# Kernel optimization log

Hardware: AMD Instinct MI355X
Metric: run time of the kernel (lower is better)

## Reference

```python
import jax, jax.numpy as jnp
import numpy as np

N_E = 1024
N_H = 16
SZ = N_E // N_H  # 64
NEG_INF = float('-inf')


def _layernorm(x, g, b):
    # Faithful to source: unbiased variance (ddof=1), eps added AFTER sqrt.
    mu = jnp.mean(x, axis=-1, keepdims=True)
    v = jnp.var(x, axis=-1, keepdims=True, ddof=1)
    xn = (x - mu) / (jnp.sqrt(v) + 1e-8)
    return g * xn + b


def setup_inputs() -> dict:
    key = jax.random.key(0)
    ks = jax.random.split(key, 16)
    s = 0.02
    x = jax.random.normal(ks[0], (4, 2048, N_E), dtype=jnp.float32)
    # Stacked per-head Q/K/V linears: weight [H, sz, n_e], bias [H, sz]
    Wq = jax.random.normal(ks[1], (N_H, SZ, N_E), dtype=jnp.float32) * s
    bq = jax.random.normal(ks[2], (N_H, SZ), dtype=jnp.float32) * s
    Wk = jax.random.normal(ks[3], (N_H, SZ, N_E), dtype=jnp.float32) * s
    bk = jax.random.normal(ks[4], (N_H, SZ), dtype=jnp.float32) * s
    Wv = jax.random.normal(ks[5], (N_H, SZ, N_E), dtype=jnp.float32) * s
    bv = jax.random.normal(ks[6], (N_H, SZ), dtype=jnp.float32) * s
    Wo = jax.random.normal(ks[7], (N_E, N_E), dtype=jnp.float32) * s
    bo = jax.random.normal(ks[8], (N_E,), dtype=jnp.float32) * s
    g1 = jnp.ones((N_E,), dtype=jnp.float32)
    be1 = jnp.zeros((N_E,), dtype=jnp.float32)
    g2 = jnp.ones((N_E,), dtype=jnp.float32)
    be2 = jnp.zeros((N_E,), dtype=jnp.float32)
    W1 = jax.random.normal(ks[9], (4 * N_E, N_E), dtype=jnp.float32) * s
    bf1 = jax.random.normal(ks[10], (4 * N_E,), dtype=jnp.float32) * s
    W2 = jax.random.normal(ks[11], (N_E, 4 * N_E), dtype=jnp.float32) * s
    bf2 = jax.random.normal(ks[12], (N_E,), dtype=jnp.float32) * s
    return dict(x=x, Wq=Wq, bq=bq, Wk=Wk, bk=bk, Wv=Wv, bv=bv, Wo=Wo, bo=bo,
                g1=g1, be1=be1, g2=g2, be2=be2, W1=W1, bf1=bf1, W2=W2, bf2=bf2)


def reference(x, Wq, bq, Wk, bk, Wv, bv, Wo, bo, g1, be1, g2, be2, W1, bf1, W2, bf2):
    # --- MHA sublayer ---
    xn = _layernorm(x, g1, be1)
    # Q/K/V for all heads at once: [B, H, S, sz]
    Q = jnp.einsum('bsd,hkd->bhsk', xn, Wq) + bq[None, :, None, :]
    K = jnp.einsum('bsd,hkd->bhsk', xn, Wk) + bk[None, :, None, :]
    V = jnp.einsum('bsd,hkd->bhsk', xn, Wv) + bv[None, :, None, :]
    scores = jnp.einsum('bhqk,bhmk->bhqm', Q, K) / (SZ ** 0.5)  # [B,H,S,S]
    # Faithful to source quirk: mask where tril(scores) == 0
    masked = jnp.where(jnp.tril(scores) == 0, NEG_INF, scores)
    attn = jax.nn.softmax(masked, axis=-1)
    o = jnp.einsum('bhqm,bhmk->bhqk', attn, V)  # [B,H,S,sz]
    B, H, S, _ = o.shape
    o = jnp.transpose(o, (0, 2, 1, 3)).reshape(B, S, H * SZ)  # concat heads
    x = x + o @ Wo.T + bo
    # --- FFN sublayer (dropout = identity in eval) ---
    xn2 = _layernorm(x, g2, be2)
    h = jax.nn.gelu(xn2 @ W1.T + bf1, approximate=False)
    x = x + h @ W2.T + bf2
    return x
```

## Files before the change

### kernel.cpp

```cpp
#include <hip/hip_runtime.h>
#include <math.h>


typedef unsigned short u16;
typedef unsigned int u32;
typedef __attribute__((ext_vector_type(8))) short bf16x8;
typedef __attribute__((ext_vector_type(4))) float f32x4;

#define T_TOK 8192
#define DM    1024
#define SEQ   2048

__device__ __forceinline__ u16 f2bf(float f) {
  union { float f; unsigned int u; } c; c.f = f;
  unsigned int u = c.u + 0x7fffu + ((c.u >> 16) & 1u);
  return (u16)(u >> 16);
}

__device__ __forceinline__ u32 pk2(float a, float b) {
  return (u32)f2bf(a) | ((u32)f2bf(b) << 16);
}

__device__ __forceinline__ float bf2f(short s) {
  union { float f; unsigned int u; } c; c.u = ((u32)(u16)s) << 16;
  return c.f;
}

__device__ __forceinline__ void gload16(const void* gp, void* lp) {
  __builtin_amdgcn_global_load_lds(
      (const __attribute__((address_space(1))) void*)gp,
      (__attribute__((address_space(3))) void*)lp, 16, 0, 0);
}

__global__ __launch_bounds__(256) void cast_all(const float* __restrict__ Wq,
    const float* __restrict__ Wk, const float* __restrict__ Wv,
    const float* __restrict__ Wo, const float* __restrict__ W1,
    const float* __restrict__ W2, u16* __restrict__ WqkvB,
    u16* __restrict__ WoB, u16* __restrict__ W1B, u16* __restrict__ W2B) {
  for (int i = blockIdx.x * 256 + threadIdx.x; i < 3145728; i += gridDim.x * 256) {
    const float* s; u16* d; int j;
    if (i < 262144)       { s = Wq; d = WqkvB;           j = i; }
    else if (i < 524288)  { s = Wk; d = WqkvB + 1048576; j = i - 262144; }
    else if (i < 786432)  { s = Wv; d = WqkvB + 2097152; j = i - 524288; }
    else if (i < 1048576) { s = Wo; d = WoB;             j = i - 786432; }
    else if (i < 2097152) { s = W1; d = W1B;             j = i - 1048576; }
    else                  { s = W2; d = W2B;             j = i - 2097152; }
    float4 v = reinterpret_cast<const float4*>(s)[j];
    ushort4 o = { f2bf(v.x), f2bf(v.y), f2bf(v.z), f2bf(v.w) };
    reinterpret_cast<ushort4*>(d)[j] = o;
  }
}

__global__ __launch_bounds__(256) void concat_bias(const float* __restrict__ q,
    const float* __restrict__ k, const float* __restrict__ v, float* __restrict__ out) {
  int i = blockIdx.x * 256 + threadIdx.x;
  float val = (i < 1024) ? q[i] : (i < 2048) ? k[i - 1024] : v[i - 2048];
  out[i] = val;
}

__global__ __launch_bounds__(256) void ln_kernel(const float* __restrict__ x,
    const float* __restrict__ g, const float* __restrict__ b, u16* __restrict__ out) {
  __shared__ float red[4];
  const int tid = threadIdx.x, l = tid & 63, w = tid >> 6;
  const size_t row = blockIdx.x;
  float4 v = reinterpret_cast<const float4*>(x + row * DM)[tid];
  float s = v.x + v.y + v.z + v.w;
#pragma unroll
  for (int off = 1; off < 64; off <<= 1) s += __shfl_xor(s, off, 64);
  if (l == 0) red[w] = s;
  __syncthreads();
  float mu = (red[0] + red[1] + red[2] + red[3]) * (1.0f / 1024.0f);
  float dx = v.x - mu, dy = v.y - mu, dz = v.z - mu, dw = v.w - mu;
  float ss = dx * dx + dy * dy + dz * dz + dw * dw;
#pragma unroll
  for (int off = 1; off < 64; off <<= 1) ss += __shfl_xor(ss, off, 64);
  __syncthreads();
  if (l == 0) red[w] = ss;
  __syncthreads();
  float var = (red[0] + red[1] + red[2] + red[3]) * (1.0f / 1023.0f);
  float inv = 1.0f / (sqrtf(var) + 1e-8f);
  const int c = tid * 4;
  u16* o = out + row * DM + c;
  o[0] = f2bf(dx * inv * g[c + 0] + b[c + 0]);
  o[1] = f2bf(dy * inv * g[c + 1] + b[c + 1]);
  o[2] = f2bf(dz * inv * g[c + 2] + b[c + 2]);
  o[3] = f2bf(dw * inv * g[c + 3] + b[c + 3]);
}

__global__ __launch_bounds__(256) void vt_kernel(const u16* __restrict__ vr,
                                                 u16* __restrict__ vt) {
  __shared__ u16 t[64][72];
  const int st = blockIdx.x;
  const int bh = blockIdx.y, b = bh >> 4, h = bh & 15;
  const int tid = threadIdx.x;
  const int ss = tid >> 3, dc = (tid & 7) * 8;
  const u16* src = vr + (size_t)(b * SEQ + st * 64) * 1024 + h * 64;
  *(bf16x8*)&t[ss][dc]      = *(const bf16x8*)(src + (size_t)ss * 1024 + dc);
  *(bf16x8*)&t[ss + 32][dc] = *(const bf16x8*)(src + (size_t)(ss + 32) * 1024 + dc);
  __syncthreads();
  const int d0 = tid >> 3, s0 = (tid & 7) * 8;
  u16* dst = vt + (size_t)bh * 64 * SEQ + st * 64;
  bf16x8 o0, o1;
#pragma unroll
  for (int i = 0; i < 8; ++i) {
    o0[i] = (short)t[s0 + i][d0];
    o1[i] = (short)t[s0 + i][d0 + 32];
  }
  *(bf16x8*)(dst + (size_t)d0 * SEQ + s0)        = o0;
  *(bf16x8*)(dst + (size_t)(d0 + 32) * SEQ + s0) = o1;
}

template <int EPI, int BM>
__global__ __launch_bounds__(512) void gemm8p(const u16* __restrict__ A,
    const u16* __restrict__ Bw, const float* __restrict__ bias,
    const float* res, void* Cout, void* aux, int M, int N, int K, int gx) {
  constexpr int MI  = BM / 32;
  constexpr int AMI = MI / 2;
  constexpr int VC  = (BM == 256) ? 6 : 5;
  __shared__ __align__(16) u16 ldsA[2][2][BM * 32];
  __shared__ __align__(16) u16 ldsB[2][2][256 * 32];
  const int tid = threadIdx.x;
  const int l = tid & 63;
  const int w = tid >> 6;
  const int wm = w >> 2, wn = w & 3;
  const int lr = l & 15, lg = l >> 4;

  const int nb = gridDim.x;
  const int q = nb >> 3, r = nb & 7;
  const int xcd = blockIdx.x & 7, jj = blockIdx.x >> 3;
  const int lid = (xcd < r ? xcd * (q + 1) : r * (q + 1) + (xcd - r) * q) + jj;
  const int stid = lid >> 5, pos = lid & 31;
  const int nstx = gx >> 2;
  const int stx = stid % nstx, sty = stid / nstx;
  const int bx = stx * 4 + (pos & 3), by = sty * 8 + (pos >> 2);
  const int m0 = by * BM, n0 = bx * 256;

  const int Dl = tid * 16;
  const int Ls = Dl ^ (((Dl >> 7) & 3) << 4);
  const int srow = Ls >> 6;
  const int scol = (Ls & 63) >> 1;
  const u16* aS0 = A  + (size_t)(m0 + srow) * K + scol;
  const u16* aS1 = aS0 + (size_t)128 * K;
  const u16* bS0 = Bw + (size_t)(n0 + srow) * K + scol;
  const u16* bS1 = bS0 + (size_t)128 * K;

  const int sx = ((lr >> 1) & 3) << 4;
  const int aBase = (wm * (BM / 2) + lr) * 64 + ((lg * 16) ^ sx);
  const int bBase = (wn * 64 + lr) * 64 + ((lg * 16) ^ sx);

  f32x4 acc[MI][4];
#pragma unroll
  for (int i = 0; i < MI; ++i)
#pragma unroll
    for (int j = 0; j < 4; ++j) acc[i][j] = f32x4{0.f, 0.f, 0.f, 0.f};
  bf16x8 bv[2][4];

  const int NT = K >> 6;
  const int NI = NT >> 1;

  auto stA = [&](int d, int ks, int tile) {
    u16* dst = &ldsA[d][ks][tid * 8];
    const int ko = tile * 64 + ks * 32;
    gload16(aS0 + ko, dst);
    if constexpr (BM == 256) gload16(aS1 + ko, dst + 4096);
  };
  auto stB = [&](int d, int ks, int tile) {
    u16* dst = &ldsB[d][ks][tid * 8];
    const int ko = tile * 64 + ks * 32;
    gload16(bS0 + ko, dst);
    gload16(bS1 + ko, dst + 4096);
  };

  stB(0, 0, 0); stB(0, 1, 0); stA(0, 0, 0); stA(0, 1, 0);
  stB(1, 0, 1); stB(1, 1, 1); stA(1, 0, 1);
  asm volatile("s_waitcnt vmcnt(%0)" :: "i"(VC) : "memory");
  __builtin_amdgcn_sched_barrier(0);
  __builtin_amdgcn_s_barrier();

#define PHASE(DBUF, KS, MH, READB, STAGE, ENDV)                               \
  {                                                                           \
    const char* abuf = (const char*)&ldsA[DBUF][KS][0];                       \
    const char* bbuf = (const char*)&ldsB[DBUF][KS][0];                       \
    bf16x8 av[AMI];                                                           \
    _Pragma("unroll")                                                         \
    for (int i = 0; i < AMI; ++i)                                             \
      av[i] = *(const bf16x8*)(abuf + aBase + ((MH) * AMI + i) * 1024);       \
    if (READB) {                                                              \
      _Pragma("unroll")                                                       \
      for (int ni = 0; ni < 4; ++ni)                                          \
        bv[KS][ni] = *(const bf16x8*)(bbuf + bBase + ni * 1024);              \
    }                                                                         \
    STAGE;                                                                    \
    __builtin_amdgcn_s_barrier();                                             \
    asm volatile("s_waitcnt lgkmcnt(0)" ::: "memory");                        \
    __builtin_amdgcn_sched_barrier(0);                                        \
    __builtin_amdgcn_s_setprio(1);                                            \
    _Pragma("unroll")                                                         \
    for (int i = 0; i < AMI; ++i)                                             \
      _Pragma("unroll")                                                       \
      for (int ni = 0; ni < 4; ++ni)                                          \
        acc[(MH) * AMI + i][ni] = __builtin_amdgcn_mfma_f32_16x16x32_bf16(    \
            av[i], bv[KS][ni], acc[(MH) * AMI + i][ni], 0, 0, 0);             \
    __builtin_amdgcn_s_setprio(0);                                            \
    ENDV;                                                                     \
    __builtin_amdgcn_s_barrier();                                             \
  }

#define ENDV_CNT                                                              \
  {                                                                           \
    if (t + 1 < NI) {                                                         \
      asm volatile("s_waitcnt vmcnt(%0)" :: "i"(VC) : "memory");              \
    } else {                                                                  \
      asm volatile("s_waitcnt vmcnt(0)" ::: "memory");                        \
    }                                                                         \
    __builtin_amdgcn_sched_barrier(0);                                        \
  }

  for (int t = 0; t < NI; ++t) {
    const int t2 = 2 * t;
    const bool s0 = (t2 + 2 < NT);
    const bool s1 = (t2 + 3 < NT);
    PHASE(0, 0, 0, 1, { stA(1, 1, t2 + 1); }, {});
    PHASE(0, 1, 0, 1, { if (s0) stB(0, 0, t2 + 2); }, {});
    PHASE(0, 0, 1, 0, { if (s0) stB(0, 1, t2 + 2); }, {});
    PHASE(0, 1, 1, 0, { if (s0) stA(0, 0, t2 + 2); }, ENDV_CNT);
    PHASE(1, 0, 0, 1, { if (s0) stA(0, 1, t2 + 2); }, {});
    PHASE(1, 1, 0, 1, { if (s1) stB(1, 0, t2 + 3); }, {});
    PHASE(1, 0, 1, 0, { if (s1) stB(1, 1, t2 + 3); }, {});
    PHASE(1, 1, 1, 0, { if (s1) stA(1, 0, t2 + 3); }, ENDV_CNT);
  }
#undef PHASE
#undef ENDV_CNT

  float bs[4];
#pragma unroll
  for (int ni = 0; ni < 4; ++ni) bs[ni] = bias[n0 + wn * 64 + ni * 16 + lr];
#pragma unroll
  for (int mi = 0; mi < MI; ++mi) {
#pragma unroll
    for (int j = 0; j < 4; ++j) {
      const int rr = m0 + wm * (BM / 2) + mi * 16 + lg * 4 + j;
#pragma unroll
      for (int ni = 0; ni < 4; ++ni) {
        const int c = n0 + wn * 64 + ni * 16 + lr;
        float v = acc[mi][ni][j] + bs[ni];
        if constexpr (EPI == 0) {
          if (n0 >= 2048) {
            ((u16*)aux)[(size_t)rr * 1024 + (c - 2048)] = f2bf(v);
          } else {
            ((u16*)Cout)[(size_t)rr * 2048 + c] = f2bf(v);
          }
        } else if constexpr (EPI == 1) {
          const size_t idx = (size_t)rr * N + c;
          ((float*)Cout)[idx] = v + res[idx];
        } else {
          const size_t idx = (size_t)rr * N + c;
          float gv = 0.5f * v * (1.0f + erff(v * 0.70710678118654752f));
          ((u16*)Cout)[idx] = f2bf(gv);
        }
      }
    }
  }
}

__global__ __launch_bounds__(512) void attn_kernel(const u16* __restrict__ qk,
    const u16* __restrict__ vt, u16* __restrict__ obuf) {
  __shared__ __align__(16) u16 ldsK[64 * 64];
  __shared__ __align__(16) u16 ldsV[64 * 64];
  __shared__ __align__(16) u16 ldsP[8][2][16 * 72];
  const int tid = threadIdx.x, l = tid & 63, w = tid >> 6;
  const int lr = l & 15, lg = l >> 4;
  const int bx = blockIdx.x;
  const int bh = blockIdx.y, b = bh >> 4, h = bh & 15;
  const u16* qbase = qk + (size_t)b * SEQ * 2048 + h * 64;
  const u16* kbase = qk + (size_t)b * SEQ * 2048 + 1024 + h * 64;
  const u16* vbase = vt + (size_t)bh * 64 * SEQ;

  const int srow = tid >> 3;
  const int scb  = ((tid & 7) * 16) ^ ((srow & 7) << 4);
  const int sel  = scb >> 1;

#pragma unroll
  for (int half = 0; half < 2; ++half) {
    const int qt = half ? (7 - bx) : bx;
    const int q0 = qt * 256 + w * 32;
    bf16x8 qf[2][2];
#pragma unroll
    for (int mi = 0; mi < 2; ++mi)
#pragma unroll
      for (int ks = 0; ks < 2; ++ks) {
        bf16x8 raw = *(const bf16x8*)(qbase +
            (size_t)(q0 + mi * 16 + lr) * 2048 + ks * 32 + lg * 8);
        bf16x8 sc8;
#pragma unroll
        for (int i = 0; i < 8; ++i) sc8[i] = (short)f2bf(bf2f(raw[i]) * 0.125f);
        qf[mi][ks] = sc8;
      }

    f32x4 o[2][4];
#pragma unroll
    for (int mi = 0; mi < 2; ++mi)
#pragma unroll
      for (int nd = 0; nd < 4; ++nd) o[mi][nd] = f32x4{0.f, 0.f, 0.f, 0.f};
    float m_[2] = {-1e30f, -1e30f}, ls[2] = {0.f, 0.f};

    const int nt = 4 * qt + 4;
    const int qmaxw = q0 + 31;

    for (int kt = 0; kt < nt; ++kt) {
      gload16(kbase + (size_t)(kt * 64 + srow) * 2048 + sel, &ldsK[tid * 8]);
      gload16(vbase + (size_t)srow * SEQ + kt * 64 + sel,    &ldsV[tid * 8]);
      __syncthreads();

      if (kt * 64 <= qmaxw) {
        f32x4 sc[2][4];
#pragma unroll
        for (int mi = 0; mi < 2; ++mi)
#pragma unroll
          for (int ni = 0; ni < 4; ++ni) sc[mi][ni] = f32x4{0.f, 0.f, 0.f, 0.f};
#pragma unroll
        for (int ks = 0; ks < 2; ++ks)
#pragma unroll
          for (int ni = 0; ni < 4; ++ni) {
            const int r2 = ni * 16 + lr;
            const int cb = (r2 << 7) + ((ks * 64 + lg * 16) ^ ((r2 & 7) << 4));
            bf16x8 kf = *(const bf16x8*)&ldsK[cb >> 1];
            sc[0][ni] = __builtin_amdgcn_mfma_f32_16x16x32_bf16(kf, qf[0][ks], sc[0][ni], 0, 0, 0);
            sc[1][ni] = __builtin_amdgcn_mfma_f32_16x16x32_bf16(kf, qf[1][ks], sc[1][ni], 0, 0, 0);
          }

        if (kt * 64 + 63 > q0) {
#pragma unroll
          for (int mi = 0; mi < 2; ++mi) {
            const int qa = q0 + mi * 16 + lr;
#pragma unroll
            for (int ni = 0; ni < 4; ++ni)
#pragma unroll
              for (int j = 0; j < 4; ++j) {
                const int ka = kt * 64 + ni * 16 + lg * 4 + j;
                if (ka > qa) sc[mi][ni][j] = -1e30f;
              }
          }
        }

#pragma unroll
        for (int mi = 0; mi < 2; ++mi) {
          float mx = sc[mi][0][0];
#pragma unroll
          for (int ni = 0; ni < 4; ++ni)
#pragma unroll
            for (int j = 0; j < 4; ++j) mx = fmaxf(mx, sc[mi][ni][j]);
          mx = fmaxf(mx, __shfl_xor(mx, 16, 64));
          mx = fmaxf(mx, __shfl_xor(mx, 32, 64));
          const float newm = fmaxf(m_[mi], mx);
          const float alpha = __expf(m_[mi] - newm);
          m_[mi] = newm;
          float ps = 0.f;
#pragma unroll
          for (int ni = 0; ni < 4; ++ni) {
            float p0 = __expf(sc[mi][ni][0] - newm);
            float p1 = __expf(sc[mi][ni][1] - newm);
            float p2 = __expf(sc[mi][ni][2] - newm);
            float p3 = __expf(sc[mi][ni][3] - newm);
            ps += (p0 + p1) + (p2 + p3);
            u32 w0 = pk2(p0, p1), w1 = pk2(p2, p3);
            *(uint2*)&ldsP[w][mi][lr * 72 + ni * 16 + lg * 4] = make_uint2(w0, w1);
          }
          ps += __shfl_xor(ps, 16, 64);
          ps += __shfl_xor(ps, 32, 64);
          ls[mi] = ls[mi] * alpha + ps;
          const float a0 = __shfl(alpha, lg * 4 + 0, 16);
          const float a1 = __shfl(alpha, lg * 4 + 1, 16);
          const float a2 = __shfl(alpha, lg * 4 + 2, 16);
          const float a3 = __shfl(alpha, lg * 4 + 3, 16);
#pragma unroll
          for (int nd = 0; nd < 4; ++nd) {
            o[mi][nd][0] *= a0; o[mi][nd][1] *= a1;
            o[mi][nd][2] *= a2; o[mi][nd][3] *= a3;
          }
        }

#pragma unroll
        for (int ks = 0; ks < 2; ++ks) {
          bf16x8 pf0 = *(const bf16x8*)&ldsP[w][0][lr * 72 + ks * 32 + lg * 8];
          bf16x8 pf1 = *(const bf16x8*)&ldsP[w][1][lr * 72 + ks * 32 + lg * 8];
#pragma unroll
          for (int nd = 0; nd < 4; ++nd) {
            const int r2 = nd * 16 + lr;
            const int cb = (r2 << 7) + ((ks * 64 + lg * 16) ^ ((r2 & 7) << 4));
            bf16x8 vf = *(const bf16x8*)&ldsV[cb >> 1];
            o[0][nd] = __builtin_amdgcn_mfma_f32_16x16x32_bf16(pf0, vf, o[0][nd], 0, 0, 0);
            o[1][nd] = __builtin_amdgcn_mfma_f32_16x16x32_bf16(pf1, vf, o[1][nd], 0, 0, 0);
          }
        }
      }
      __syncthreads();
    }

#pragma unroll
    for (int mi = 0; mi < 2; ++mi) {
      const float i0 = 1.0f / __shfl(ls[mi], lg * 4 + 0, 16);
      const float i1 = 1.0f / __shfl(ls[mi], lg * 4 + 1, 16);
      const float i2 = 1.0f / __shfl(ls[mi], lg * 4 + 2, 16);
      const float i3 = 1.0f / __shfl(ls[mi], lg * 4 + 3, 16);
      const int qrow = q0 + mi * 16 + lg * 4;
#pragma unroll
      for (int nd = 0; nd < 4; ++nd) {
        const int d = nd * 16 + lr;
        u16* op = obuf + (size_t)(b * SEQ + qrow) * DM + h * 64 + d;
        op[0 * DM] = f2bf(o[mi][nd][0] * i0);
        op[1 * DM] = f2bf(o[mi][nd][1] * i1);
        op[2 * DM] = f2bf(o[mi][nd][2] * i2);
        op[3 * DM] = f2bf(o[mi][nd][3] * i3);
      }
    }
  }
}

extern "C" void kernel_launch(void* const* d_in, const int* in_sizes, int n_in,
                              void* d_out, int out_size, void* d_ws, size_t ws_size,
                              hipStream_t stream) {
  const float* x   = (const float*)d_in[0];
  const float* Wq  = (const float*)d_in[1];
  const float* bq  = (const float*)d_in[2];
  const float* Wk  = (const float*)d_in[3];
  const float* bk  = (const float*)d_in[4];
  const float* Wv  = (const float*)d_in[5];
  const float* bv  = (const float*)d_in[6];
  const float* Wo  = (const float*)d_in[7];
  const float* bo  = (const float*)d_in[8];
  const float* g1  = (const float*)d_in[9];
  const float* be1 = (const float*)d_in[10];
  const float* g2  = (const float*)d_in[11];
  const float* be2 = (const float*)d_in[12];
  const float* W1  = (const float*)d_in[13];
  const float* bf1 = (const float*)d_in[14];
  const float* W2  = (const float*)d_in[15];
  const float* bf2 = (const float*)d_in[16];
  float* out = (float*)d_out;

  char* ws = (char*)d_ws;
  size_t off = 0;
  auto alloc = [&](size_t bytes) {
    char* p = ws + off;
    off += (bytes + 255) & ~(size_t)255;
    return p;
  };
  u16* xnB = (u16*)alloc((size_t)T_TOK * DM * 2);
  u16* D    = (u16*)alloc((size_t)T_TOK * 4096 * 2);
  u16* qkB  = D;
  u16* VTg  = D + (size_t)T_TOK * 2048;
  u16* Vrow = D + (size_t)T_TOK * 3072;
  u16* oB   = Vrow;
  u16* HB   = D;
  u16*   WqkvB = (u16*)alloc((size_t)3072 * 1024 * 2);
  u16*   WoB   = (u16*)alloc((size_t)1024 * 1024 * 2);
  u16*   W1B   = (u16*)alloc((size_t)4096 * 1024 * 2);
  u16*   W2B   = (u16*)alloc((size_t)1024 * 4096 * 2);
  float* bqkv  = (float*)alloc(3072 * 4);

  cast_all<<<2048, 256, 0, stream>>>(Wq, Wk, Wv, Wo, W1, W2,
                                     WqkvB, WoB, W1B, W2B);
  concat_bias<<<12, 256, 0, stream>>>(bq, bk, bv, bqkv);

  ln_kernel<<<T_TOK, 256, 0, stream>>>(x, g1, be1, xnB);
  gemm8p<0, 256><<<384, 512, 0, stream>>>(xnB, WqkvB, bqkv, nullptr,
                                          qkB, Vrow, T_TOK, 3072, 1024, 12);
  vt_kernel<<<dim3(32, 64), 256, 0, stream>>>(Vrow, VTg);
  attn_kernel<<<dim3(4, 64), 512, 0, stream>>>(qkB, VTg, oB);
  gemm8p<1, 128><<<256, 512, 0, stream>>>(oB, WoB, bo, x,
                                          out, nullptr, T_TOK, 1024, 1024, 4);

  ln_kernel<<<T_TOK, 256, 0, stream>>>(out, g2, be2, xnB);
  gemm8p<2, 256><<<512, 512, 0, stream>>>(xnB, W1B, bf1, nullptr,
                                          HB, nullptr, T_TOK, 4096, 1024, 16);
  gemm8p<1, 128><<<256, 512, 0, stream>>>(HB, W2B, bf2, out,
                                          out, nullptr, T_TOK, 1024, 4096, 4);
}
```

Before: 418.6 us.

## Triple-buffer K/V tiles in attention and use tanh GELU approximation

After: 396.4 us. -5.3%, faster.

```diff
diff --git a/kernel.cpp b/kernel.cpp
--- a/kernel.cpp
+++ b/kernel.cpp
@@ -30,6 +30,11 @@
   __builtin_amdgcn_global_load_lds(
       (const __attribute__((address_space(1))) void*)gp,
       (__attribute__((address_space(3))) void*)lp, 16, 0, 0);
+}
+
+__device__ __forceinline__ float gelu_tanh(float v) {
+  float u = 0.7978845608f * (v + 0.044715f * v * v * v);
+  return v / (1.0f + __expf(-2.0f * u));
 }
 
 __global__ __launch_bounds__(256) void cast_all(const float* __restrict__ Wq,
@@ -255,8 +260,7 @@
           ((float*)Cout)[idx] = v + res[idx];
         } else {
           const size_t idx = (size_t)rr * N + c;
-          float gv = 0.5f * v * (1.0f + erff(v * 0.70710678118654752f));
-          ((u16*)Cout)[idx] = f2bf(gv);
+          ((u16*)Cout)[idx] = f2bf(gelu_tanh(v));
         }
       }
     }
@@ -265,8 +269,8 @@
 
 __global__ __launch_bounds__(512) void attn_kernel(const u16* __restrict__ qk,
     const u16* __restrict__ vt, u16* __restrict__ obuf) {
-  __shared__ __align__(16) u16 ldsK[64 * 64];
-  __shared__ __align__(16) u16 ldsV[64 * 64];
+  __shared__ __align__(16) u16 ldsK[3][64 * 64];
+  __shared__ __align__(16) u16 ldsV[3][64 * 64];
   __shared__ __align__(16) u16 ldsP[8][2][16 * 72];
   const int tid = threadIdx.x, l = tid & 63, w = tid >> 6;
   const int lr = l & 15, lg = l >> 4;
@@ -280,6 +284,12 @@
   const int scb  = ((tid & 7) * 16) ^ ((srow & 7) << 4);
   const int sel  = scb >> 1;
 
+  auto stageKV = [&](int t) {
+    const int bi = t % 3;
+    gload16(kbase + (size_t)(t * 64 + srow) * 2048 + sel, &ldsK[bi][tid * 8]);
+    gload16(vbase + (size_t)srow * SEQ + t * 64 + sel,    &ldsV[bi][tid * 8]);
+  };
+
 #pragma unroll
   for (int half = 0; half < 2; ++half) {
     const int qt = half ? (7 - bx) : bx;
@@ -307,10 +317,19 @@
     const int nt = 4 * qt + 4;
     const int qmaxw = q0 + 31;
 
+    stageKV(0);
+
     for (int kt = 0; kt < nt; ++kt) {
-      gload16(kbase + (size_t)(kt * 64 + srow) * 2048 + sel, &ldsK[tid * 8]);
-      gload16(vbase + (size_t)srow * SEQ + kt * 64 + sel,    &ldsV[tid * 8]);
-      __syncthreads();
+      if (kt + 1 < nt) {
+        stageKV(kt + 1);
+        asm volatile("s_waitcnt vmcnt(2)" ::: "memory");
+      } else {
+        asm volatile("s_waitcnt vmcnt(0)" ::: "memory");
+      }
+      __builtin_amdgcn_s_barrier();
+      __builtin_amdgcn_sched_barrier(0);
+      const u16* bK = &ldsK[kt % 3][0];
+      const u16* bV = &ldsV[kt % 3][0];
 
       if (kt * 64 <= qmaxw) {
         f32x4 sc[2][4];
@@ -324,7 +343,7 @@
           for (int ni = 0; ni < 4; ++ni) {
             const int r2 = ni * 16 + lr;
             const int cb = (r2 << 7) + ((ks * 64 + lg * 16) ^ ((r2 & 7) << 4));
-            bf16x8 kf = *(const bf16x8*)&ldsK[cb >> 1];
+            bf16x8 kf = *(const bf16x8*)&bK[cb >> 1];
             sc[0][ni] = __builtin_amdgcn_mfma_f32_16x16x32_bf16(kf, qf[0][ks], sc[0][ni], 0, 0, 0);
             sc[1][ni] = __builtin_amdgcn_mfma_f32_16x16x32_bf16(kf, qf[1][ks], sc[1][ni], 0, 0, 0);
           }
@@ -388,14 +407,14 @@
           for (int nd = 0; nd < 4; ++nd) {
             const int r2 = nd * 16 + lr;
             const int cb = (r2 << 7) + ((ks * 64 + lg * 16) ^ ((r2 & 7) << 4));
-            bf16x8 vf = *(const bf16x8*)&ldsV[cb >> 1];
+            bf16x8 vf = *(const bf16x8*)&bV[cb >> 1];
             o[0][nd] = __builtin_amdgcn_mfma_f32_16x16x32_bf16(pf0, vf, o[0][nd], 0, 0, 0);
             o[1][nd] = __builtin_amdgcn_mfma_f32_16x16x32_bf16(pf1, vf, o[1][nd], 0, 0, 0);
           }
         }
       }
-      __syncthreads();
     }
+    __builtin_amdgcn_s_barrier();
 
 #pragma unroll
     for (int mi = 0; mi < 2; ++mi) {
```
